# Performance work log

Hardware: AMD Instinct MI355X
Metric: run time of the kernel (lower is better)

The kernel has to match this reference:

```python
import jax, jax.numpy as jnp
import numpy as np

TRUST_W, SIM_W, STALE_W = 0.4, 0.4, 0.2
EPS = 1e-8  # torch cosine_similarity norm clamp


def setup_inputs() -> dict:
    key = jax.random.key(0)
    ks = jax.random.split(key, 6)
    B, D, E, C = 8192, 1024, 32, 256
    x = jax.random.normal(ks[0], (B, D), dtype=jnp.float32)
    expert_features = jax.random.normal(ks[1], (E, D), dtype=jnp.float32)
    trust = jax.random.uniform(ks[2], (E,), dtype=jnp.float32)
    staleness = jax.random.uniform(ks[3], (E,), dtype=jnp.float32)
    W = jax.random.normal(ks[4], (E, C, D), dtype=jnp.float32) * 0.02
    b = jax.random.normal(ks[5], (E, C), dtype=jnp.float32) * 0.02
    return {"x": x, "expert_features": expert_features, "trust": trust,
            "staleness": staleness, "W": W, "b": b, "k": 4}


def reference(x, expert_features, trust, staleness, W, b, k):
    # --- scoring: trust + cosine similarity + staleness, per (token, expert) ---
    xn = x / jnp.maximum(jnp.linalg.norm(x, axis=-1, keepdims=True), EPS)
    efn = expert_features / jnp.maximum(
        jnp.linalg.norm(expert_features, axis=-1, keepdims=True), EPS)
    cos = xn @ efn.T                              # [B, E]
    sim = (cos + 1.0) * 0.5
    stale_score = jnp.maximum(0.0, 1.0 - staleness)  # [E]
    scores = TRUST_W * trust + SIM_W * sim + STALE_W * stale_score  # [B, E]

    # --- top-k expert selection per token ---
    _, idx = jax.lax.top_k(scores, k)             # [B, k] int32

    # --- grouped expert heads: dense all-expert GEMM, then gather top-k ---
    all_out = jnp.einsum('bd,ecd->bec', x, W) + b  # [B, E, C]
    sel = jnp.take_along_axis(all_out, idx[:, :, None], axis=1)  # [B, k, C]
    return sel.mean(axis=1)                        # [B, C]
```

## Files before the change

### kernel.cpp

```cpp
#include <hip/hip_runtime.h>
#include <math.h>

#define KMAX 8
#define CSTRIDE 64

typedef short s16x8 __attribute__((ext_vector_type(8)));
typedef float f32x4 __attribute__((ext_vector_type(4)));

__device__ inline ushort f2bf(float f) {
    union { float f; unsigned u; } v; v.f = f;
    unsigned r = v.u + 0x7fffu + ((v.u >> 16) & 1u);
    return (ushort)(r >> 16);
}
__device__ inline float bf2f(ushort b) {
    union { unsigned u; float f; } v; v.u = ((unsigned)b) << 16; return v.f;
}

__device__ inline void gload_lds16(const void* g, void* l) {
    __builtin_amdgcn_global_load_lds(
        (const __attribute__((address_space(1))) unsigned int*)g,
        (__attribute__((address_space(3))) unsigned int*)l, 16, 0, 0);
}

__global__ void k_efnorm(const float* __restrict__ ef, int D,
                         double* __restrict__ efn) {
    int e = blockIdx.x;
    int lane = threadIdx.x;
    double s = 0.0;
    for (int i = lane; i < D; i += 64) {
        double v = (double)ef[(size_t)e * D + i];
        s = fma(v, v, s);
    }
    #pragma unroll
    for (int off = 32; off > 0; off >>= 1) s += __shfl_xor(s, off);
    if (lane == 0) efn[e] = sqrt(s);
}

__global__ __launch_bounds__(256) void k_prep_w(
    const float* __restrict__ W, const int* __restrict__ counts,
    int perExpF4, ushort* __restrict__ wbf, int* __restrict__ offs) {
    int e = blockIdx.y;
    if (blockIdx.x == 0 && e == 0 && threadIdx.x == 0) {
        int s = 0;
        for (int e2 = 0; e2 < 32; ++e2) { offs[e2] = s; s += counts[e2 * CSTRIDE]; }
    }
    if (counts[e * CSTRIDE] == 0) return;
    size_t base = (size_t)e * perExpF4;
    #pragma unroll
    for (int j = 0; j < 4; ++j) {
        int idx = (blockIdx.x * 4 + j) * 256 + threadIdx.x;
        if (idx < perExpF4) {
            float4 v = *(const float4*)&W[(base + idx) * 4];
            ushort4 u;
            u.x = f2bf(v.x); u.y = f2bf(v.y); u.z = f2bf(v.z); u.w = f2bf(v.w);
            *(ushort4*)&wbf[(base + idx) * 4] = u;
        }
    }
}

__global__ __launch_bounds__(256) void k_scores3(
    const float* __restrict__ x, const float* __restrict__ ef,
    const float* __restrict__ trust, const float* __restrict__ stale,
    const double* __restrict__ efn, const int* __restrict__ kp,
    int D, int B, ushort* __restrict__ xbf,
    int* __restrict__ counts, int* __restrict__ lists, int* __restrict__ sel)
{
    __shared__ float xs[16 * 64];
    __shared__ float efs[32 * 64];
    __shared__ double sc[16 * 33];
    __shared__ int bcnt[32];
    __shared__ int bbase[32];
    __shared__ unsigned char selb[16 * KMAX];
    __shared__ unsigned char lposb[16 * KMAX];

    int tid = threadIdx.x;
    int tp = tid >> 4, eg = tid & 15;
    int tb = blockIdx.x * 16;

    if (tid < 32) bcnt[tid] = 0;

    int rx = tid >> 4, qx = tid & 15;
    int re0 = tid >> 4, re1 = 16 + (tid >> 4);
    int qe = tid & 15;

    int nch = D / 64;

    float4 vx  = *(const float4*)&x[(size_t)(tb + rx) * D + qx * 4];
    float4 ve0 = *(const float4*)&ef[(size_t)re0 * D + qe * 4];
    float4 ve1 = *(const float4*)&ef[(size_t)re1 * D + qe * 4];

    double acc0 = 0.0, acc1 = 0.0, axx = 0.0;

    for (int ch = 0; ch < nch; ++ch) {
        *(float4*)&xs[rx * 64 + ((qx ^ rx) << 2)] = vx;
        {
            ushort4 u;
            u.x = f2bf(vx.x); u.y = f2bf(vx.y); u.z = f2bf(vx.z); u.w = f2bf(vx.w);
            *(ushort4*)&xbf[(size_t)(tb + rx) * D + ch * 64 + qx * 4] = u;
        }
        *(float4*)&efs[re0 * 64 + ((qe ^ (re0 & 15)) << 2)] = ve0;
        *(float4*)&efs[re1 * 64 + ((qe ^ (re1 & 15)) << 2)] = ve1;
        __syncthreads();

        if (ch + 1 < nch) {
            int k1 = (ch + 1) * 64;
            vx  = *(const float4*)&x[(size_t)(tb + rx) * D + k1 + qx * 4];
            ve0 = *(const float4*)&ef[(size_t)re0 * D + k1 + qe * 4];
            ve1 = *(const float4*)&ef[(size_t)re1 * D + k1 + qe * 4];
        }

        float a0 = 0.f, a1 = 0.f, ax = 0.f;
        #pragma unroll
        for (int q = 0; q < 16; ++q) {
            float4 xv = *(const float4*)&xs[tp * 64 + ((q ^ tp) << 2)];
            float4 e0 = *(const float4*)&efs[eg * 64 + ((q ^ eg) << 2)];
            float4 e1 = *(const float4*)&efs[(eg + 16) * 64 + ((q ^ eg) << 2)];
            a0 = fmaf(xv.x, e0.x, a0); a0 = fmaf(xv.y, e0.y, a0);
            a0 = fmaf(xv.z, e0.z, a0); a0 = fmaf(xv.w, e0.w, a0);
            a1 = fmaf(xv.x, e1.x, a1); a1 = fmaf(xv.y, e1.y, a1);
            a1 = fmaf(xv.z, e1.z, a1); a1 = fmaf(xv.w, e1.w, a1);
            ax = fmaf(xv.x, xv.x, ax); ax = fmaf(xv.y, xv.y, ax);
            ax = fmaf(xv.z, xv.z, ax); ax = fmaf(xv.w, xv.w, ax);
        }
        __syncthreads();
        acc0 += (double)a0; acc1 += (double)a1; axx += (double)ax;
    }

    double xn = fmax(sqrt(axx), 1e-8);
    {
        int e0i = eg;
        double en0 = fmax(efn[e0i], 1e-8);
        sc[tp * 33 + e0i] = 0.4 * (double)trust[e0i]
            + 0.2 * (acc0 / (xn * en0) + 1.0)
            + 0.2 * fmax(0.0, 1.0 - (double)stale[e0i]);
        int e1i = eg + 16;
        double en1 = fmax(efn[e1i], 1e-8);
        sc[tp * 33 + e1i] = 0.4 * (double)trust[e1i]
            + 0.2 * (acc1 / (xn * en1) + 1.0)
            + 0.2 * fmax(0.0, 1.0 - (double)stale[e1i]);
    }
    __syncthreads();

    int kk = kp[0]; kk = kk < 1 ? 1 : (kk > KMAX ? KMAX : kk);

    if (tid < 16) {
        unsigned mask = 0;
        for (int p = 0; p < kk; ++p) {
            double bv = -1e300; int be = 0;
            #pragma unroll
            for (int e = 0; e < 32; ++e) {
                double v = sc[tid * 33 + e];
                if (!((mask >> e) & 1u) && v > bv) { bv = v; be = e; }
            }
            mask |= 1u << be;
            selb[tid * KMAX + p] = (unsigned char)be;
            lposb[tid * KMAX + p] = (unsigned char)atomicAdd(&bcnt[be], 1);
        }
    }
    __syncthreads();
    if (tid < 32) {
        int c = bcnt[tid];
        bbase[tid] = c ? atomicAdd(&counts[tid * CSTRIDE], c) : 0;
    }
    __syncthreads();
    if (tid < 16) {
        int t = tb + tid;
        for (int p = 0; p < kk; ++p) {
            int e = selb[tid * KMAX + p];
            int pos = bbase[e] + lposb[tid * KMAX + p];
            lists[(size_t)e * B + pos] = t;
            sel[(size_t)t * KMAX + p] = (e << 24) | pos;
        }
    }
}

__global__ __launch_bounds__(512) void k_moe3(
    const ushort* __restrict__ xbf, const ushort* __restrict__ wbf,
    const float* __restrict__ bias, const int* __restrict__ lists,
    const int* __restrict__ counts, const int* __restrict__ offs,
    const int* __restrict__ kp, int B, int C, int D,
    int usePart, ushort* __restrict__ part, float* __restrict__ out)
{
    int e = blockIdx.z;
    int cnt = counts[e * CSTRIDE];
    int row0 = blockIdx.x * 128;
    if (row0 >= cnt) return;
    int col0 = blockIdx.y * 128;
    int nt = min(128, cnt - row0);

    __shared__ ushort xs[128 * 64];
    __shared__ ushort wsh[128 * 64];
    __shared__ int toks[128];

    int tid = threadIdx.x;
    if (tid < 128) toks[tid] = (tid < nt) ? lists[(size_t)e * B + row0 + tid] : 0;
    __syncthreads();

    int lane = tid & 63, wid = tid >> 6;
    int wr = wid >> 1, wc = wid & 1;
    int l15 = lane & 15, l16 = lane >> 4;

    f32x4 acc[2][4];
    #pragma unroll
    for (int m = 0; m < 2; ++m)
        #pragma unroll
        for (int n = 0; n < 4; ++n) acc[m][n] = (f32x4){0.f, 0.f, 0.f, 0.f};

    int nch = D / 64;
    for (int ch = 0; ch < nch; ++ch) {
        int k0 = ch * 64;
        #pragma unroll
        for (int t = 0; t < 2; ++t) {
            int id = t * 512 + tid;
            int r = id >> 3, seg = id & 7;
            int ssw = (seg ^ (r & 7)) << 3;
            gload_lds16(&xbf[(size_t)toks[r] * D + k0 + ssw],
                        (char*)xs + (size_t)(t * 512 + wid * 64) * 16);
        }
        #pragma unroll
        for (int t = 0; t < 2; ++t) {
            int id = t * 512 + tid;
            int r = id >> 3, seg = id & 7;
            int ssw = (seg ^ (r & 7)) << 3;
            gload_lds16(&wbf[((size_t)e * C + col0 + r) * D + k0 + ssw],
                        (char*)wsh + (size_t)(t * 512 + wid * 64) * 16);
        }
        __syncthreads();
        #pragma unroll
        for (int ks = 0; ks < 2; ++ks) {
            s16x8 a[2], bfr[4];
            int sbase = ks * 4 + l16;
            #pragma unroll
            for (int m = 0; m < 2; ++m) {
                int r = wr * 32 + m * 16 + l15;
                a[m] = *(const s16x8*)&xs[r * 64 + ((sbase ^ (l15 & 7)) << 3)];
            }
            #pragma unroll
            for (int n = 0; n < 4; ++n) {
                int r = wc * 64 + n * 16 + l15;
                bfr[n] = *(const s16x8*)&wsh[r * 64 + ((sbase ^ (l15 & 7)) << 3)];
            }
            #pragma unroll
            for (int m = 0; m < 2; ++m)
                #pragma unroll
                for (int n = 0; n < 4; ++n)
                    acc[m][n] = __builtin_amdgcn_mfma_f32_16x16x32_bf16(
                        a[m], bfr[n], acc[m][n], 0, 0, 0);
        }
        __syncthreads();
    }

    int kk = kp[0]; kk = kk < 1 ? 1 : (kk > KMAX ? KMAX : kk);
    if (usePart) {
        int slotBase = offs[e] + row0;
        #pragma unroll
        for (int m = 0; m < 2; ++m) {
            int rbase = wr * 32 + m * 16 + l16 * 4;
            #pragma unroll
            for (int n = 0; n < 4; ++n) {
                int col = col0 + wc * 64 + n * 16 + l15;
                float bv = bias[(size_t)e * C + col];
                #pragma unroll
                for (int r = 0; r < 4; ++r) {
                    int rl = rbase + r;
                    if (rl < nt)
                        part[(size_t)(slotBase + rl) * C + col] =
                            f2bf(acc[m][n][r] + bv);
                }
            }
        }
    } else {
        float invk = 1.0f / (float)kk;
        #pragma unroll
        for (int m = 0; m < 2; ++m) {
            int rbase = wr * 32 + m * 16 + l16 * 4;
            #pragma unroll
            for (int n = 0; n < 4; ++n) {
                int col = col0 + wc * 64 + n * 16 + l15;
                float bv = bias[(size_t)e * C + col];
                #pragma unroll
                for (int r = 0; r < 4; ++r) {
                    int rl = rbase + r;
                    if (rl < nt)
                        atomicAdd(&out[(size_t)toks[rl] * C + col],
                                  invk * (acc[m][n][r] + bv));
                }
            }
        }
    }
}

__global__ __launch_bounds__(256) void k_combine(
    const ushort* __restrict__ part, const int* __restrict__ sel,
    const int* __restrict__ offs, const int* __restrict__ kp,
    int C, float* __restrict__ out)
{
    int kk = kp[0]; kk = kk < 1 ? 1 : (kk > KMAX ? KMAX : kk);
    float invk = 1.0f / (float)kk;
    int sub = threadIdx.x >> 6, lane = threadIdx.x & 63;
    int t = blockIdx.x * 4 + sub;
    for (int c = lane * 4; c < C; c += 256) {
        float s0 = 0.f, s1 = 0.f, s2 = 0.f, s3 = 0.f;
        for (int p = 0; p < kk; ++p) {
            int sv = sel[(size_t)t * KMAX + p];
            int slot = offs[sv >> 24] + (sv & 0xFFFFFF);
            ushort4 u = *(const ushort4*)&part[(size_t)slot * C + c];
            s0 += bf2f(u.x); s1 += bf2f(u.y); s2 += bf2f(u.z); s3 += bf2f(u.w);
        }
        float4 o = make_float4(invk * s0, invk * s1, invk * s2, invk * s3);
        *(float4*)&out[(size_t)t * C + c] = o;
    }
}

__global__ __launch_bounds__(256) void k_scores_legacy(
    const float* __restrict__ x, const float* __restrict__ ef,
    const float* __restrict__ trust, const float* __restrict__ stale,
    const double* __restrict__ efn, const int* __restrict__ kp,
    int D, int B, int* __restrict__ counts, int* __restrict__ lists)
{
    __shared__ float xs[32][72];
    __shared__ float efs[32][72];
    __shared__ double sc[32][33];

    int tid = threadIdx.x;
    int tl = tid >> 3, eg = tid & 7;
    int tb = blockIdx.x * 32;

    double acc[4] = {0, 0, 0, 0};
    double axx = 0.0;
    int nch = D / 64;

    for (int ch = 0; ch < nch; ++ch) {
        #pragma unroll
        for (int t = 0; t < 2; ++t) {
            int id = t * 256 + tid;
            int r = id >> 4, q = id & 15;
            float4 v = *(const float4*)&x[(size_t)(tb + r) * D + ch * 64 + q * 4];
            *(float4*)&xs[r][q * 4] = v;
            float4 w = *(const float4*)&ef[(size_t)r * D + ch * 64 + q * 4];
            *(float4*)&efs[r][q * 4] = w;
        }
        __syncthreads();
        #pragma unroll 4
        for (int q = 0; q < 16; ++q) {
            float4 xv = *(const float4*)&xs[tl][q * 4];
            double x0 = xv.x, x1 = xv.y, x2 = xv.z, x3 = xv.w;
            axx = fma(x0, x0, fma(x1, x1, fma(x2, x2, fma(x3, x3, axx))));
            #pragma unroll
            for (int j = 0; j < 4; ++j) {
                float4 ev = *(const float4*)&efs[eg + 8 * j][q * 4];
                acc[j] = fma(x0, (double)ev.x, acc[j]);
                acc[j] = fma(x1, (double)ev.y, acc[j]);
                acc[j] = fma(x2, (double)ev.z, acc[j]);
                acc[j] = fma(x3, (double)ev.w, acc[j]);
            }
        }
        __syncthreads();
    }

    double xn = fmax(sqrt(axx), 1e-8);
    #pragma unroll
    for (int j = 0; j < 4; ++j) {
        int e = eg + 8 * j;
        double en = fmax(efn[e], 1e-8);
        double cosv = acc[j] / (xn * en);
        sc[tl][e] = 0.4 * (double)trust[e] + 0.2 * (cosv + 1.0)
                  + 0.2 * fmax(0.0, 1.0 - (double)stale[e]);
    }
    __syncthreads();

    if (tid < 32) {
        int kk = kp[0]; kk = kk < 1 ? 1 : (kk > KMAX ? KMAX : kk);
        unsigned mask = 0;
        int t = tb + tid;
        for (int p = 0; p < kk; ++p) {
            double bv = -1e300; int be = 0;
            #pragma unroll
            for (int e = 0; e < 32; ++e) {
                double v = sc[tid][e];
                if (!((mask >> e) & 1u) && v > bv) { bv = v; be = e; }
            }
            mask |= 1u << be;
            int pos = atomicAdd(&counts[be * CSTRIDE], 1);
            lists[(size_t)be * B + pos] = t;
        }
    }
}

__global__ __launch_bounds__(512) void k_moe_f32(
    const float* __restrict__ x, const float* __restrict__ W,
    const float* __restrict__ bias, const int* __restrict__ lists,
    const int* __restrict__ counts, const int* __restrict__ kp,
    int B, int C, int D, float* __restrict__ out)
{
    int e = blockIdx.z;
    int cnt = counts[e * CSTRIDE];
    int row0 = blockIdx.x * 128;
    if (row0 >= cnt) return;
    int col0 = blockIdx.y * 256;
    int nt = min(128, cnt - row0);

    __shared__ ushort xs[128 * 72];
    __shared__ ushort wsh[256 * 72];
    __shared__ int toks[128];

    int tid = threadIdx.x;
    if (tid < 128) toks[tid] = (tid < nt) ? lists[(size_t)e * B + row0 + tid] : 0;
    __syncthreads();

    int lane = tid & 63, wid = tid >> 6;
    int wr = wid >> 2, wc = wid & 3;
    int l15 = lane & 15, l16 = lane >> 4;

    f32x4 acc[4][4];
    #pragma unroll
    for (int m = 0; m < 4; ++m)
        #pragma unroll
        for (int n = 0; n < 4; ++n) acc[m][n] = (f32x4){0.f, 0.f, 0.f, 0.f};

    int nch = D / 64;
    for (int ch = 0; ch < nch; ++ch) {
        int k0 = ch * 64;
        #pragma unroll
        for (int t = 0; t < 4; ++t) {
            int id = t * 512 + tid;
            int r = id >> 4, q = id & 15;
            float4 v = (r < nt)
                ? *(const float4*)&x[(size_t)toks[r] * D + k0 + q * 4]
                : make_float4(0.f, 0.f, 0.f, 0.f);
            ushort4 u;
            u.x = f2bf(v.x); u.y = f2bf(v.y); u.z = f2bf(v.z); u.w = f2bf(v.w);
            *(ushort4*)&xs[r * 72 + q * 4] = u;
        }
        #pragma unroll
        for (int t = 0; t < 8; ++t) {
            int id = t * 512 + tid;
            int r = id >> 4, q = id & 15;
            float4 v = *(const float4*)&W[((size_t)e * C + col0 + r) * D + k0 + q * 4];
            ushort4 u;
            u.x = f2bf(v.x); u.y = f2bf(v.y); u.z = f2bf(v.z); u.w = f2bf(v.w);
            *(ushort4*)&wsh[r * 72 + q * 4] = u;
        }
        __syncthreads();
        #pragma unroll
        for (int ks = 0; ks < 2; ++ks) {
            s16x8 a[4], bfr[4];
            #pragma unroll
            for (int m = 0; m < 4; ++m)
                a[m] = *(const s16x8*)&xs[(wr * 64 + m * 16 + l15) * 72 + ks * 32 + l16 * 8];
            #pragma unroll
            for (int n = 0; n < 4; ++n)
                bfr[n] = *(const s16x8*)&wsh[(wc * 64 + n * 16 + l15) * 72 + ks * 32 + l16 * 8];
            #pragma unroll
            for (int m = 0; m < 4; ++m)
                #pragma unroll
                for (int n = 0; n < 4; ++n)
                    acc[m][n] = __builtin_amdgcn_mfma_f32_16x16x32_bf16(
                        a[m], bfr[n], acc[m][n], 0, 0, 0);
        }
        __syncthreads();
    }

    int kk = kp[0]; kk = kk < 1 ? 1 : (kk > KMAX ? KMAX : kk);
    float invk = 1.0f / (float)kk;
    #pragma unroll
    for (int m = 0; m < 4; ++m) {
        int rbase = wr * 64 + m * 16 + l16 * 4;
        #pragma unroll
        for (int n = 0; n < 4; ++n) {
            int col = col0 + wc * 64 + n * 16 + l15;
            float bv = bias[(size_t)e * C + col];
            #pragma unroll
            for (int r = 0; r < 4; ++r) {
                int rl = rbase + r;
                if (rl < nt)
                    atomicAdd(&out[(size_t)toks[rl] * C + col],
                              invk * (acc[m][n][r] + bv));
            }
        }
    }
}

extern "C" void kernel_launch(void* const* d_in, const int* in_sizes, int n_in,
                              void* d_out, int out_size, void* d_ws, size_t ws_size,
                              hipStream_t stream) {
    const float* x     = (const float*)d_in[0];
    const float* ef    = (const float*)d_in[1];
    const float* trust = (const float*)d_in[2];
    const float* stale = (const float*)d_in[3];
    const float* W     = (const float*)d_in[4];
    const float* b     = (const float*)d_in[5];
    const int*   kp    = (const int*)d_in[6];

    int E = in_sizes[2];
    int D = in_sizes[1] / E;
    int B = in_sizes[0] / D;
    int C = in_sizes[5] / E;
    float* out = (float*)d_out;

    char* ws = (char*)d_ws;
    double* efn   = (double*)ws;
    int*    counts= (int*)(ws + 256);
    size_t off_offs = 256 + 32 * CSTRIDE * 4;
    int*    offs  = (int*)(ws + off_offs);
    size_t off_sel = off_offs + 256;
    int*    sel   = (int*)(ws + off_sel);
    size_t off_lists = off_sel + (size_t)B * KMAX * 4;
    int*    lists = (int*)(ws + off_lists);
    size_t off_xbf = off_lists + (size_t)E * B * 4;
    off_xbf = (off_xbf + 255) & ~(size_t)255;
    ushort* xbf = (ushort*)(ws + off_xbf);
    size_t off_wbf = off_xbf + (size_t)B * D * 2;
    ushort* wbf = (ushort*)(ws + off_wbf);
    size_t off_part = off_wbf + (size_t)E * C * D * 2;
    off_part = (off_part + 255) & ~(size_t)255;
    ushort* part = (ushort*)(ws + off_part);
    size_t need_mid  = off_part;
    size_t need_full = off_part + (size_t)B * KMAX * C * 2;

    bool fullPath = ws_size >= need_mid;
    int usePart = (fullPath && ws_size >= need_full) ? 1 : 0;

    hipMemsetAsync(counts, 0, 32 * CSTRIDE * 4, stream);
    if (!usePart)
        hipMemsetAsync(d_out, 0, (size_t)out_size * sizeof(float), stream);

    k_efnorm<<<E, 64, 0, stream>>>(ef, D, efn);

    if (fullPath) {
        k_scores3<<<B / 16, 256, 0, stream>>>(x, ef, trust, stale, efn,
                                              kp, D, B, xbf, counts, lists, sel);
        int perExpF4 = (C * D) / 4;
        dim3 wgrid((perExpF4 + 1023) / 1024, E);
        k_prep_w<<<wgrid, 256, 0, stream>>>(W, counts, perExpF4, wbf, offs);
        dim3 grid((B + 127) / 128, C / 128, E);
        k_moe3<<<grid, 512, 0, stream>>>(xbf, wbf, b, lists, counts, offs, kp,
                                         B, C, D, usePart, part, out);
        if (usePart)
            k_combine<<<B / 4, 256, 0, stream>>>(part, sel, offs, kp, C, out);
    } else {
        k_scores_legacy<<<B / 32, 256, 0, stream>>>(x, ef, trust, stale, efn,
                                                    kp, D, B, counts, lists);
        dim3 grid((B + 127) / 128, C / 256, E);
        k_moe_f32<<<grid, 512, 0, stream>>>(x, W, b, lists, counts, kp,
                                            B, C, D, out);
    }
}
```

Baseline: 88.67 us.

## Fuse scoring, expert-norm and weight conversion into one launch

Removes the separate expert-norm kernel by computing expert feature norms inside the scoring loop, and appends the W-to-bf16 conversion as extra blocks of the scoring kernel so both run concurrently in one launch. The offs prefix array is dropped; moe and combine recompute per-expert offsets from counts. This cuts two kernel launches and lets weight conversion overlap scoring. In exchange it converts all experts' weights unconditionally (the old kernel skipped experts with zero count), and every scoring thread does extra FMAs for the norms in float rather than double.

```diff
diff --git a/kernel.cpp b/kernel.cpp
--- a/kernel.cpp
+++ b/kernel.cpp
@@ -22,47 +22,12 @@
         (__attribute__((address_space(3))) unsigned int*)l, 16, 0, 0);
 }
 
-__global__ void k_efnorm(const float* __restrict__ ef, int D,
-                         double* __restrict__ efn) {
-    int e = blockIdx.x;
-    int lane = threadIdx.x;
-    double s = 0.0;
-    for (int i = lane; i < D; i += 64) {
-        double v = (double)ef[(size_t)e * D + i];
-        s = fma(v, v, s);
-    }
-    #pragma unroll
-    for (int off = 32; off > 0; off >>= 1) s += __shfl_xor(s, off);
-    if (lane == 0) efn[e] = sqrt(s);
-}
-
-__global__ __launch_bounds__(256) void k_prep_w(
-    const float* __restrict__ W, const int* __restrict__ counts,
-    int perExpF4, ushort* __restrict__ wbf, int* __restrict__ offs) {
-    int e = blockIdx.y;
-    if (blockIdx.x == 0 && e == 0 && threadIdx.x == 0) {
-        int s = 0;
-        for (int e2 = 0; e2 < 32; ++e2) { offs[e2] = s; s += counts[e2 * CSTRIDE]; }
-    }
-    if (counts[e * CSTRIDE] == 0) return;
-    size_t base = (size_t)e * perExpF4;
-    #pragma unroll
-    for (int j = 0; j < 4; ++j) {
-        int idx = (blockIdx.x * 4 + j) * 256 + threadIdx.x;
-        if (idx < perExpF4) {
-            float4 v = *(const float4*)&W[(base + idx) * 4];
-            ushort4 u;
-            u.x = f2bf(v.x); u.y = f2bf(v.y); u.z = f2bf(v.z); u.w = f2bf(v.w);
-            *(ushort4*)&wbf[(base + idx) * 4] = u;
-        }
-    }
-}
-
-__global__ __launch_bounds__(256) void k_scores3(
+__global__ __launch_bounds__(256) void k_fused(
     const float* __restrict__ x, const float* __restrict__ ef,
     const float* __restrict__ trust, const float* __restrict__ stale,
-    const double* __restrict__ efn, const int* __restrict__ kp,
-    int D, int B, ushort* __restrict__ xbf,
+    const float* __restrict__ W, const int* __restrict__ kp,
+    int D, int B, int C, int nSB, int bpe,
+    ushort* __restrict__ xbf, ushort* __restrict__ wbf,
     int* __restrict__ counts, int* __restrict__ lists, int* __restrict__ sel)
 {
     __shared__ float xs[16 * 64];
@@ -74,6 +39,26 @@
     __shared__ unsigned char lposb[16 * KMAX];
 
     int tid = threadIdx.x;
+
+    if ((int)blockIdx.x >= nSB) {
+        int wb = blockIdx.x - nSB;
+        int e = wb / bpe, sub = wb % bpe;
+        int perExpF4 = (C * D) / 4;
+        size_t base = (size_t)e * perExpF4;
+        #pragma unroll
+        for (int j = 0; j < 4; ++j) {
+            int idx = (sub * 4 + j) * 256 + tid;
+            if (idx < perExpF4) {
+                float4 v = *(const float4*)&W[(base + idx) * 4];
+                ushort4 u;
+                u.x = f2bf(v.x); u.y = f2bf(v.y);
+                u.z = f2bf(v.z); u.w = f2bf(v.w);
+                *(ushort4*)&wbf[(base + idx) * 4] = u;
+            }
+        }
+        return;
+    }
+
     int tp = tid >> 4, eg = tid & 15;
     int tb = blockIdx.x * 16;
 
@@ -90,6 +75,7 @@
     float4 ve1 = *(const float4*)&ef[(size_t)re1 * D + qe * 4];
 
     double acc0 = 0.0, acc1 = 0.0, axx = 0.0;
+    double nacc0 = 0.0, nacc1 = 0.0;
 
     for (int ch = 0; ch < nch; ++ch) {
         *(float4*)&xs[rx * 64 + ((qx ^ rx) << 2)] = vx;
@@ -109,7 +95,7 @@
             ve1 = *(const float4*)&ef[(size_t)re1 * D + k1 + qe * 4];
         }
 
-        float a0 = 0.f, a1 = 0.f, ax = 0.f;
+        float a0 = 0.f, a1 = 0.f, ax = 0.f, n0 = 0.f, n1 = 0.f;
         #pragma unroll
         for (int q = 0; q < 16; ++q) {
             float4 xv = *(const float4*)&xs[tp * 64 + ((q ^ tp) << 2)];
@@ -121,20 +107,25 @@
             a1 = fmaf(xv.z, e1.z, a1); a1 = fmaf(xv.w, e1.w, a1);
             ax = fmaf(xv.x, xv.x, ax); ax = fmaf(xv.y, xv.y, ax);
             ax = fmaf(xv.z, xv.z, ax); ax = fmaf(xv.w, xv.w, ax);
+            n0 = fmaf(e0.x, e0.x, n0); n0 = fmaf(e0.y, e0.y, n0);
+            n0 = fmaf(e0.z, e0.z, n0); n0 = fmaf(e0.w, e0.w, n0);
+            n1 = fmaf(e1.x, e1.x, n1); n1 = fmaf(e1.y, e1.y, n1);
+            n1 = fmaf(e1.z, e1.z, n1); n1 = fmaf(e1.w, e1.w, n1);
         }
         __syncthreads();
         acc0 += (double)a0; acc1 += (double)a1; axx += (double)ax;
+        nacc0 += (double)n0; nacc1 += (double)n1;
     }
 
     double xn = fmax(sqrt(axx), 1e-8);
     {
         int e0i = eg;
-        double en0 = fmax(efn[e0i], 1e-8);
+        double en0 = fmax(sqrt(nacc0), 1e-8);
         sc[tp * 33 + e0i] = 0.4 * (double)trust[e0i]
             + 0.2 * (acc0 / (xn * en0) + 1.0)
             + 0.2 * fmax(0.0, 1.0 - (double)stale[e0i]);
         int e1i = eg + 16;
-        double en1 = fmax(efn[e1i], 1e-8);
+        double en1 = fmax(sqrt(nacc1), 1e-8);
         sc[tp * 33 + e1i] = 0.4 * (double)trust[e1i]
             + 0.2 * (acc1 / (xn * en1) + 1.0)
             + 0.2 * fmax(0.0, 1.0 - (double)stale[e1i]);
@@ -177,9 +168,9 @@
 __global__ __launch_bounds__(512) void k_moe3(
     const ushort* __restrict__ xbf, const ushort* __restrict__ wbf,
     const float* __restrict__ bias, const int* __restrict__ lists,
-    const int* __restrict__ counts, const int* __restrict__ offs,
-    const int* __restrict__ kp, int B, int C, int D,
-    int usePart, ushort* __restrict__ part, float* __restrict__ out)
+    const int* __restrict__ counts, const int* __restrict__ kp,
+    int B, int C, int D, int usePart,
+    ushort* __restrict__ part, float* __restrict__ out)
 {
     int e = blockIdx.z;
     int cnt = counts[e * CSTRIDE];
@@ -252,7 +243,9 @@
 
     int kk = kp[0]; kk = kk < 1 ? 1 : (kk > KMAX ? KMAX : kk);
     if (usePart) {
-        int slotBase = offs[e] + row0;
+        int offE = 0;
+        for (int e2 = 0; e2 < e; ++e2) offE += counts[e2 * CSTRIDE];
+        int slotBase = offE + row0;
         #pragma unroll
         for (int m = 0; m < 2; ++m) {
             int rbase = wr * 32 + m * 16 + l16 * 4;
@@ -292,24 +285,44 @@
 
 __global__ __launch_bounds__(256) void k_combine(
     const ushort* __restrict__ part, const int* __restrict__ sel,
-    const int* __restrict__ offs, const int* __restrict__ kp,
+    const int* __restrict__ counts, const int* __restrict__ kp,
     int C, float* __restrict__ out)
 {
     int kk = kp[0]; kk = kk < 1 ? 1 : (kk > KMAX ? KMAX : kk);
     float invk = 1.0f / (float)kk;
     int sub = threadIdx.x >> 6, lane = threadIdx.x & 63;
     int t = blockIdx.x * 4 + sub;
+    int slot[KMAX];
+    for (int p = 0; p < kk; ++p) {
+        int sv = sel[(size_t)t * KMAX + p];
+        int e = sv >> 24;
+        int offE = 0;
+        for (int e2 = 0; e2 < e; ++e2) offE += counts[e2 * CSTRIDE];
+        slot[p] = offE + (sv & 0xFFFFFF);
+    }
     for (int c = lane * 4; c < C; c += 256) {
         float s0 = 0.f, s1 = 0.f, s2 = 0.f, s3 = 0.f;
         for (int p = 0; p < kk; ++p) {
-            int sv = sel[(size_t)t * KMAX + p];
-            int slot = offs[sv >> 24] + (sv & 0xFFFFFF);
-            ushort4 u = *(const ushort4*)&part[(size_t)slot * C + c];
+            ushort4 u = *(const ushort4*)&part[(size_t)slot[p] * C + c];
             s0 += bf2f(u.x); s1 += bf2f(u.y); s2 += bf2f(u.z); s3 += bf2f(u.w);
         }
         float4 o = make_float4(invk * s0, invk * s1, invk * s2, invk * s3);
         *(float4*)&out[(size_t)t * C + c] = o;
     }
+}
+
+__global__ void k_efnorm(const float* __restrict__ ef, int D,
+                         double* __restrict__ efn) {
+    int e = blockIdx.x;
+    int lane = threadIdx.x;
+    double s = 0.0;
+    for (int i = lane; i < D; i += 64) {
+        double v = (double)ef[(size_t)e * D + i];
+        s = fma(v, v, s);
+    }
+    #pragma unroll
+    for (int off = 32; off > 0; off >>= 1) s += __shfl_xor(s, off);
+    if (lane == 0) efn[e] = sqrt(s);
 }
 
 __global__ __launch_bounds__(256) void k_scores_legacy(
@@ -501,9 +514,7 @@
     char* ws = (char*)d_ws;
     double* efn   = (double*)ws;
     int*    counts= (int*)(ws + 256);
-    size_t off_offs = 256 + 32 * CSTRIDE * 4;
-    int*    offs  = (int*)(ws + off_offs);
-    size_t off_sel = off_offs + 256;
+    size_t off_sel = 256 + 32 * CSTRIDE * 4 + 256;
     int*    sel   = (int*)(ws + off_sel);
     size_t off_lists = off_sel + (size_t)B * KMAX * 4;
     int*    lists = (int*)(ws + off_lists);
@@ -525,20 +536,20 @@
     if (!usePart)
         hipMemsetAsync(d_out, 0, (size_t)out_size * sizeof(float), stream);
 
-    k_efnorm<<<E, 64, 0, stream>>>(ef, D, efn);
-
     if (fullPath) {
-        k_scores3<<<B / 16, 256, 0, stream>>>(x, ef, trust, stale, efn,
-                                              kp, D, B, xbf, counts, lists, sel);
-        int perExpF4 = (C * D) / 4;
-        dim3 wgrid((perExpF4 + 1023) / 1024, E);
-        k_prep_w<<<wgrid, 256, 0, stream>>>(W, counts, perExpF4, wbf, offs);
+        int nSB = B / 16;
+        int bpe = ((C * D) / 4 + 1023) / 1024;
+        int nWB = E * bpe;
+        k_fused<<<nSB + nWB, 256, 0, stream>>>(
+            x, ef, trust, stale, W, kp, D, B, C, nSB, bpe,
+            xbf, wbf, counts, lists, sel);
         dim3 grid((B + 127) / 128, C / 128, E);
-        k_moe3<<<grid, 512, 0, stream>>>(xbf, wbf, b, lists, counts, offs, kp,
+        k_moe3<<<grid, 512, 0, stream>>>(xbf, wbf, b, lists, counts, kp,
                                          B, C, D, usePart, part, out);
         if (usePart)
-            k_combine<<<B / 4, 256, 0, stream>>>(part, sel, offs, kp, C, out);
+            k_combine<<<B / 4, 256, 0, stream>>>(part, sel, counts, kp, C, out);
     } else {
+        k_efnorm<<<E, 64, 0, stream>>>(ef, D, efn);
         k_scores_legacy<<<B / 32, 256, 0, stream>>>(x, ef, trust, stale, efn,
                                                     kp, D, B, counts, lists);
         dim3 grid((B + 127) / 128, C / 256, E);
```

Result: slower. 93.55 us (+5.5%).
